# Optimization experiments

Hardware: AMD Instinct MI355X
Metric: run time of the kernel (lower is better)

## Reference

```python
import jax, jax.numpy as jnp
import numpy as np

B, S, H, NH, DH, I, C, P = 4, 1024, 1280, 20, 64, 5120, 13, 8
LN_EPS = 1e-5


def setup_inputs() -> dict:
    key = jax.random.key(0)
    ks = jax.random.split(key, 20)
    n = lambda k, shp, s=0.02: (jax.random.normal(k, shp, jnp.float32) * s)
    return {
        "hidden_states": jax.random.normal(ks[0], (B, S, H), jnp.float32),
        "attention_mask": jnp.ones((B, S), jnp.float32),
        "Wq": n(ks[1], (H, H)), "bq": jnp.zeros((H,), jnp.float32),
        "Wk": n(ks[2], (H, H)), "bk": jnp.zeros((H,), jnp.float32),
        "Wv": n(ks[3], (H, H)), "bv": jnp.zeros((H,), jnp.float32),
        "W_ct1": n(ks[4], (P, C), 0.3), "b_ct1": jnp.zeros((P,), jnp.float32),
        "W_ct2": n(ks[5], (P, C), 0.3), "b_ct2": jnp.zeros((P,), jnp.float32),
        "M": n(ks[6], (C, C), 0.5),
        "bias_scale": jnp.full((1,), 0.5, jnp.float32),
        "W_ptm": n(ks[7], (P, H)), "b_ptm": jnp.zeros((P,), jnp.float32),
        "ln_g": jnp.ones((H,), jnp.float32), "ln_b": jnp.zeros((H,), jnp.float32),
        "Wf1": n(ks[8], (I, H)), "bf1": jnp.zeros((I,), jnp.float32),
        "Wf2": n(ks[9], (H, I)), "bf2": jnp.zeros((H,), jnp.float32),
    }


def reference(hidden_states, attention_mask, Wq, bq, Wk, bk, Wv, bv,
              W_ct1, b_ct1, W_ct2, b_ct2, M, bias_scale, W_ptm, b_ptm,
              ln_g, ln_b, Wf1, bf1, Wf2, bf2):
    h = hidden_states
    # crosstalk bilinear projection: (P,C) @ (C,P) -> (P,P)
    out1 = (M.T @ W_ct1.T + b_ct1).T          # (P, C)
    out2 = M @ W_ct2.T + b_ct2                # (C, P)
    R = out1 @ out2                           # (P, P)
    # ptm_predictor (Linear H->P) + softmax
    ptm = jax.nn.softmax(h @ W_ptm.T + b_ptm, axis=-1)            # (B,S,P)
    Bb = jnp.tanh(jnp.einsum('blc,cd,bmd->blm', ptm, R, ptm)) * bias_scale  # (B,S,S)
    # manual multi-head attention
    q = (h @ Wq.T + bq).reshape(B, S, NH, DH).transpose(0, 2, 1, 3)
    k = (h @ Wk.T + bk).reshape(B, S, NH, DH).transpose(0, 2, 1, 3)
    v = (h @ Wv.T + bv).reshape(B, S, NH, DH).transpose(0, 2, 1, 3)
    scores = jnp.einsum('bhld,bhmd->bhlm', q, k) / np.float32(np.sqrt(DH))
    scores = scores + Bb[:, None]
    scores = scores + (1.0 - attention_mask)[:, None, None, :] * jnp.finfo(h.dtype).min
    probs = jax.nn.softmax(scores, axis=-1)
    ctx = jnp.einsum('bhlm,bhmd->bhld', probs, v)
    ctx = ctx.transpose(0, 2, 1, 3).reshape(B, S, H)
    # residual + LayerNorm
    x = h + ctx
    mu = jnp.mean(x, -1, keepdims=True)
    var = jnp.var(x, -1, keepdims=True)
    x = (x - mu) * jax.lax.rsqrt(var + LN_EPS) * ln_g + ln_b
    # FFN with exact GELU, residual
    ff = jax.nn.gelu(x @ Wf1.T + bf1, approximate=False) @ Wf2.T + bf2
    return x + ff
```

## Files before the change

### kernel.cpp

```cpp
#include <hip/hip_runtime.h>
#include <math.h>

typedef _Float16 f16;
typedef _Float16 f16x2 __attribute__((ext_vector_type(2)));
typedef _Float16 f16x8 __attribute__((ext_vector_type(8)));
typedef _Float16 f16x4 __attribute__((ext_vector_type(4)));
typedef float f32x4 __attribute__((ext_vector_type(4)));

#define B_ 4
#define S_ 1024
#define H_ 1280
#define NH_ 20
#define DH_ 64
#define I_ 5120
#define C_ 13
#define P_ 8
#define LOG2E 1.44269504088896f

__device__ __forceinline__ void store_val(float* p, float v) { *p = v; }
__device__ __forceinline__ void store_val(f16* p, float v) { *p = (f16)v; }

__global__ __launch_bounds__(256) void cvt6_kernel(
    const float* __restrict__ s0, f16* __restrict__ d0, int n0,
    const float* __restrict__ s1, f16* __restrict__ d1, int n1,
    const float* __restrict__ s2, f16* __restrict__ d2, int n2,
    const float* __restrict__ s3, f16* __restrict__ d3, int n3,
    const float* __restrict__ s4, f16* __restrict__ d4, int n4,
    const float* __restrict__ s5, f16* __restrict__ d5, int n5) {
    int seg = blockIdx.y;
    const float* src = (seg == 0) ? s0 : (seg == 1) ? s1 : (seg == 2) ? s2
                     : (seg == 3) ? s3 : (seg == 4) ? s4 : s5;
    f16* dst = (seg == 0) ? d0 : (seg == 1) ? d1 : (seg == 2) ? d2
             : (seg == 3) ? d3 : (seg == 4) ? d4 : d5;
    int n = (seg == 0) ? n0 : (seg == 1) ? n1 : (seg == 2) ? n2
          : (seg == 3) ? n3 : (seg == 4) ? n4 : n5;
    int i = blockIdx.x * 256 + threadIdx.x;
    if (i < n) {
        f32x4 v = ((const f32x4*)src)[i];
        f16x4 o;
#pragma unroll
        for (int e = 0; e < 4; e++) o[e] = (f16)v[e];
        ((f16x4*)dst)[i] = o;
    }
}

__global__ __launch_bounds__(256) void ptm_kernel(const float* __restrict__ hin,
                                                  const float* __restrict__ Wptm,
                                                  const float* __restrict__ bptm,
                                                  const float* __restrict__ Mg,
                                                  const float* __restrict__ W1,
                                                  const float* __restrict__ b1,
                                                  const float* __restrict__ W2,
                                                  const float* __restrict__ b2,
                                                  float* __restrict__ ptm,
                                                  float* __restrict__ tg) {
    __shared__ float o1[P_][C_];
    __shared__ float o2[C_][P_];
    __shared__ float R[P_ * P_];
    int t = threadIdx.x;
    if (t < P_ * C_) {
        int p = t / C_, c = t % C_;
        float s = b1[p];
        for (int k = 0; k < C_; k++) s += Mg[k * C_ + c] * W1[p * C_ + k];
        o1[p][c] = s;
        int c2 = t / P_, p2 = t % P_;
        float s2 = b2[p2];
        for (int k = 0; k < C_; k++) s2 += Mg[c2 * C_ + k] * W2[p2 * C_ + k];
        o2[c2][p2] = s2;
    }
    __syncthreads();
    if (t < P_ * P_) {
        int p = t >> 3, q = t & 7;
        float s = 0.f;
        for (int c = 0; c < C_; c++) s += o1[p][c] * o2[c][q];
        R[t] = s;
    }
    __syncthreads();

    int wv = t >> 6, lane = t & 63;
    int row = blockIdx.x * 4 + wv;
    const float* hrow = hin + (size_t)row * H_;
    float acc[P_] = {};
    for (int i = 0; i < H_ / 64; i++) {
        int k = lane + 64 * i;
        float hv = hrow[k];
#pragma unroll
        for (int p = 0; p < P_; p++) acc[p] += hv * Wptm[p * H_ + k];
    }
#pragma unroll
    for (int p = 0; p < P_; p++) {
#pragma unroll
        for (int o = 32; o >= 1; o >>= 1) acc[p] += __shfl_xor(acc[p], o);
        acc[p] += bptm[p];
    }
    float mx = acc[0];
#pragma unroll
    for (int p = 1; p < P_; p++) mx = fmaxf(mx, acc[p]);
    float sum = 0.f;
#pragma unroll
    for (int p = 0; p < P_; p++) { acc[p] = expf(acc[p] - mx); sum += acc[p]; }
    float rinv = 1.f / sum;
#pragma unroll
    for (int p = 0; p < P_; p++) acc[p] *= rinv;
    float tv[P_];
#pragma unroll
    for (int d = 0; d < P_; d++) {
        float s = 0.f;
#pragma unroll
        for (int c = 0; c < P_; c++) s += acc[c] * R[c * P_ + d];
        tv[d] = s;
    }
    if (lane == 0) {
#pragma unroll
        for (int p = 0; p < P_; p++) {
            ptm[(size_t)row * P_ + p] = acc[p];
            tg[(size_t)row * P_ + p]  = tv[p];
        }
    }
}

__global__ __launch_bounds__(256) void bias_kernel(const float* __restrict__ tg,
                                                   const float* __restrict__ ptm,
                                                   const float* __restrict__ mask,
                                                   const float* __restrict__ bscale_p,
                                                   f16* __restrict__ bb) {
    const int bl = blockIdx.x;
    const int b = bl >> 10;
    const int t = threadIdx.x;
    __shared__ float tl[P_];
    if (t < P_) tl[t] = tg[(size_t)bl * P_ + t];
    __syncthreads();
    const float bscale = bscale_p[0];
    float t0 = tl[0], t1 = tl[1], t2 = tl[2], t3 = tl[3];
    float t4 = tl[4], t5 = tl[5], t6 = tl[6], t7 = tl[7];
#pragma unroll
    for (int i = 0; i < 4; i++) {
        int m = t + 256 * i;
        const float* pm = ptm + ((size_t)b * S_ + m) * P_;
        float4 p0 = *(const float4*)pm;
        float4 p1 = *(const float4*)(pm + 4);
        float d = t0 * p0.x + t1 * p0.y + t2 * p0.z + t3 * p0.w
                + t4 * p1.x + t5 * p1.y + t6 * p1.z + t7 * p1.w;
        float v = (tanhf(d) * bscale + (1.0f - mask[(size_t)b * S_ + m]) * (-30000.0f)) * LOG2E;
        bb[(size_t)bl * S_ + m] = (f16)v;
    }
}

template <int MODE, typename YT>
__device__ __forceinline__ void gemm_body(const f16* __restrict__ X,
                                          const f16* __restrict__ W,
                                          const float* __restrict__ bias,
                                          YT* __restrict__ Y,
                                          const f16* __restrict__ res,
                                          int Ndim, int Kdim, int kbeg, int kend,
                                          int m0, int n0, f16* sA, f16* sB) {
    const int t = threadIdx.x;
    const int lane = t & 63, w = t >> 6;
    const int wr = w >> 1, wc = w & 1;
    const int lr = lane & 15, kq = lane >> 4;

    f32x4 acc[4][4] = {};

    int s_row[4], s_gc[4];
#pragma unroll
    for (int inst = 0; inst < 4; inst++) {
        int ci = t + 256 * inst;
        s_row[inst] = ci >> 3;
        s_gc[inst] = (ci & 7) ^ (s_row[inst] & 7);
    }

    for (int k0 = kbeg; k0 < kend; k0 += 64) {
        __syncthreads();
#pragma unroll
        for (int inst = 0; inst < 4; inst++) {
            int ci = t + 256 * inst;
            __builtin_amdgcn_global_load_lds(
                (const unsigned*)(X + (size_t)(m0 + s_row[inst]) * Kdim + k0 + s_gc[inst] * 8),
                (unsigned*)(sA + ci * 8), 16, 0, 0);
        }
#pragma unroll
        for (int inst = 0; inst < 4; inst++) {
            int ci = t + 256 * inst;
            __builtin_amdgcn_global_load_lds(
                (const unsigned*)(W + (size_t)(n0 + s_row[inst]) * Kdim + k0 + s_gc[inst] * 8),
                (unsigned*)(sB + ci * 8), 16, 0, 0);
        }
        __syncthreads();
#pragma unroll
        for (int ks = 0; ks < 2; ks++) {
            f16x8 af[4], bf[4];
#pragma unroll
            for (int i = 0; i < 4; i++) {
                int row = wr * 64 + i * 16 + lr;
                int cl = (ks * 4 + kq) ^ (row & 7);
                af[i] = *(const f16x8*)(sA + row * 64 + cl * 8);
            }
#pragma unroll
            for (int j = 0; j < 4; j++) {
                int row = wc * 64 + j * 16 + lr;
                int cl = (ks * 4 + kq) ^ (row & 7);
                bf[j] = *(const f16x8*)(sB + row * 64 + cl * 8);
            }
#pragma unroll
            for (int i = 0; i < 4; i++)
#pragma unroll
                for (int j = 0; j < 4; j++)
                    acc[i][j] = __builtin_amdgcn_mfma_f32_16x16x32_f16(af[i], bf[j], acc[i][j], 0, 0, 0);
        }
    }
#pragma unroll
    for (int j = 0; j < 4; j++) {
        int col = n0 + wc * 64 + j * 16 + lr;
        float bcol = (MODE == 3) ? 0.f : bias[col];
#pragma unroll
        for (int i = 0; i < 4; i++) {
#pragma unroll
            for (int rr = 0; rr < 4; rr++) {
                int row = m0 + wr * 64 + i * 16 + kq * 4 + rr;
                float v = acc[i][j][rr] + bcol;
                if (MODE == 1) v = 0.5f * v * (1.0f + erff(v * 0.70710678118654752f));
                if (MODE == 2) v += (float)res[(size_t)row * Ndim + col];
                store_val(&Y[(size_t)row * Ndim + col], v);
            }
        }
    }
}

template <int MODE, typename YT>
__global__ __launch_bounds__(256, 2) void gemm128(const f16* __restrict__ X,
                                                  const f16* __restrict__ W,
                                                  const float* __restrict__ bias,
                                                  YT* __restrict__ Y,
                                                  const f16* __restrict__ res,
                                                  int Ndim, int Kdim) {
    __shared__ f16 sA[128 * 64];
    __shared__ f16 sB[128 * 64];
    gemm_body<MODE, YT>(X, W, bias, Y, res, Ndim, Kdim, 0, Kdim,
                        blockIdx.x * 128, blockIdx.y * 128, sA, sB);
}

__global__ __launch_bounds__(256, 2) void gemm_sk(const f16* __restrict__ X,
                                                  const f16* __restrict__ W,
                                                  float* __restrict__ Pb,
                                                  int Ndim, int Kdim, int Mdim) {
    __shared__ f16 sA[128 * 64];
    __shared__ f16 sB[128 * 64];
    const int kd2 = Kdim >> 1;
    float* Y = Pb + (size_t)blockIdx.z * Mdim * Ndim;
    gemm_body<3, float>(X, W, nullptr, Y, nullptr, Ndim, Kdim,
                        blockIdx.z * kd2, blockIdx.z * kd2 + kd2,
                        blockIdx.x * 128, blockIdx.y * 128, sA, sB);
}

__global__ __launch_bounds__(256) void reduce2_kernel(const float* __restrict__ p0,
                                                      const float* __restrict__ p1,
                                                      const float* __restrict__ bias,
                                                      const f16* __restrict__ res,
                                                      float* __restrict__ out) {
    int i = blockIdx.x * 256 + threadIdx.x;
    int col = (i * 4) % H_;
    f32x4 a = ((const f32x4*)p0)[i];
    f32x4 b = ((const f32x4*)p1)[i];
    f32x4 bc = *(const f32x4*)(bias + col);
    f16x4 r = ((const f16x4*)res)[i];
    f32x4 o;
#pragma unroll
    for (int e = 0; e < 4; e++) o[e] = a[e] + b[e] + bc[e] + (float)r[e];
    ((f32x4*)out)[i] = o;
}

__global__ __launch_bounds__(256, 2) void gemm_qkv(const f16* __restrict__ X,
                                                   const f16* __restrict__ Wq,
                                                   const f16* __restrict__ Wk,
                                                   const f16* __restrict__ Wv,
                                                   const float* __restrict__ bq,
                                                   const float* __restrict__ bk,
                                                   const float* __restrict__ bv,
                                                   f16* __restrict__ qb,
                                                   f16* __restrict__ kb,
                                                   f16* __restrict__ vb) {
    __shared__ f16 sA[128 * 64];
    __shared__ f16 sB[128 * 64];
    const int g = blockIdx.y / 10, nt = blockIdx.y % 10;
    const f16* W = (g == 0) ? Wq : (g == 1) ? Wk : Wv;
    const float* bias = (g == 0) ? bq : (g == 1) ? bk : bv;
    f16* Y = (g == 0) ? qb : (g == 1) ? kb : vb;
    gemm_body<0, f16>(X, W, bias, Y, nullptr, H_, H_, 0, H_,
                      blockIdx.x * 128, nt * 128, sA, sB);
}

__global__ __launch_bounds__(256) void attn_kernel(const f16* __restrict__ q,
                                                   const f16* __restrict__ k,
                                                   const f16* __restrict__ v,
                                                   const f16* __restrict__ bb,
                                                   const float* __restrict__ hin,
                                                   float* __restrict__ xpre) {
    __shared__ f16 sQ[64 * 72];
    __shared__ f16 sK[64 * 72];
    __shared__ f16 sVT[64 * 72];
    __shared__ f16 sP[64 * 72];

    const int t = threadIdx.x;
    const int w = t >> 6, lane = t & 63;
    const int lr = lane & 15, kq = lane >> 4;
    const int gid = blockIdx.x + 16 * (blockIdx.y + 20 * blockIdx.z);
    const int wk = (gid & 7) * 160 + (gid >> 3);
    const int l0 = (wk & 15) * 64;
    const int hb = wk >> 4;
    const int h = hb % 20, b = hb / 20;
    const size_t base = (size_t)b * S_ * H_ + (size_t)h * DH_;

    const int kr0 = t >> 3, kc8 = (t & 7) * 8;
    const int vr2 = (t >> 3) * 2, vc8 = (t & 7) * 8;
    const int vmsw = vr2 ^ vc8;

    f16x8 kA0 = *(const f16x8*)&k[base + (size_t)kr0 * H_ + kc8];
    f16x8 kA1 = *(const f16x8*)&k[base + (size_t)(kr0 + 32) * H_ + kc8];
    f16x8 vA0 = *(const f16x8*)&v[base + (size_t)vr2 * H_ + vc8];
    f16x8 vA1 = *(const f16x8*)&v[base + (size_t)(vr2 + 1) * H_ + vc8];

    for (int idx = t; idx < 512; idx += 256) {
        int r = idx >> 3, c8 = (idx & 7) * 8;
        f16x8 qv = *(const f16x8*)&q[base + (size_t)(l0 + r) * H_ + c8];
#pragma unroll
        for (int e = 0; e < 8; e++) qv[e] = (f16)((float)qv[e] * (0.125f * LOG2E));
        *(f16x8*)&sQ[r * 72 + c8] = qv;
    }
    __syncthreads();
    f16x8 afq[2];
    afq[0] = *(const f16x8*)&sQ[(w * 16 + lr) * 72 + kq * 8];
    afq[1] = *(const f16x8*)&sQ[(w * 16 + lr) * 72 + 32 + kq * 8];

    f32x4 acc_o[4] = {};
    float lstate[4] = {};

    for (int mt = 0; mt < 16; mt++) {
        const int m0 = mt * 64;
        __syncthreads();
        *(f16x8*)&sK[kr0 * 72 + kc8] = kA0;
        *(f16x8*)&sK[(kr0 + 32) * 72 + kc8] = kA1;
#pragma unroll
        for (int e = 0; e < 8; e++) {
            f16x2 pk = {vA0[e], vA1[e]};
            *(f16x2*)&sVT[(vc8 + e) * 72 + vmsw] = pk;
        }
        const int m1 = ((mt + 1) & 15) * 64;
        f16x8 kB0 = *(const f16x8*)&k[base + (size_t)(m1 + kr0) * H_ + kc8];
        f16x8 kB1 = *(const f16x8*)&k[base + (size_t)(m1 + kr0 + 32) * H_ + kc8];
        f16x8 vB0 = *(const f16x8*)&v[base + (size_t)(m1 + vr2) * H_ + vc8];
        f16x8 vB1 = *(const f16x8*)&v[base + (size_t)(m1 + vr2 + 1) * H_ + vc8];
        __syncthreads();

        f32x4 sacc[4] = {};
#pragma unroll
        for (int ks = 0; ks < 2; ks++)
#pragma unroll
            for (int j = 0; j < 4; j++) {
                f16x8 bk = *(const f16x8*)&sK[(j * 16 + lr) * 72 + ks * 32 + kq * 8];
                sacc[j] = __builtin_amdgcn_mfma_f32_16x16x32_f16(afq[ks], bk, sacc[j], 0, 0, 0);
            }
        const f16* bbrow = bb + ((size_t)b * S_ + l0 + w * 16 + kq * 4) * S_ + m0;
#pragma unroll
        for (int j = 0; j < 4; j++)
#pragma unroll
            for (int rr = 0; rr < 4; rr++)
                sacc[j][rr] += (float)bbrow[(size_t)rr * S_ + j * 16 + lr];

#pragma unroll
        for (int j = 0; j < 4; j++)
#pragma unroll
            for (int rr = 0; rr < 4; rr++) {
                float p = __builtin_exp2f(sacc[j][rr]);
                lstate[rr] += p;
                sP[(w * 16 + kq * 4 + rr) * 72 + j * 16 + lr] = (f16)p;
            }
        __syncthreads();

        f16x8 ap[2];
        ap[0] = *(const f16x8*)&sP[(w * 16 + lr) * 72 + kq * 8];
        ap[1] = *(const f16x8*)&sP[(w * 16 + lr) * 72 + 32 + kq * 8];
#pragma unroll
        for (int ks = 0; ks < 2; ks++)
#pragma unroll
            for (int j2 = 0; j2 < 4; j2++) {
                int d = j2 * 16 + lr;
                int s_ = (d >> 3) & 7;
                f16x8 bv = *(const f16x8*)&sVT[d * 72 + 8 * (((ks << 2) + kq) ^ s_)];
                acc_o[j2] = __builtin_amdgcn_mfma_f32_16x16x32_f16(ap[ks], bv, acc_o[j2], 0, 0, 0);
            }
        kA0 = kB0; kA1 = kB1; vA0 = vB0; vA1 = vB1;
    }

#pragma unroll
    for (int rr = 0; rr < 4; rr++) {
#pragma unroll
        for (int off = 8; off >= 1; off >>= 1) lstate[rr] += __shfl_xor(lstate[rr], off);
    }

#pragma unroll
    for (int rr = 0; rr < 4; rr++) {
        float linv = 1.0f / lstate[rr];
        int tok = l0 + w * 16 + kq * 4 + rr;
        size_t obase = base + (size_t)tok * H_;
#pragma unroll
        for (int j2 = 0; j2 < 4; j2++) {
            int d = j2 * 16 + lr;
            xpre[obase + d] = hin[obase + d] + acc_o[j2][rr] * linv;
        }
    }
}

__global__ __launch_bounds__(256) void ln_kernel(const float* __restrict__ xpre,
                                                 const float* __restrict__ g,
                                                 const float* __restrict__ bb,
                                                 f16* __restrict__ xln) {
    int row = blockIdx.x, t = threadIdx.x;
    const float* xr = xpre + (size_t)row * H_;
    float xv[5], s1 = 0.f, s2 = 0.f;
#pragma unroll
    for (int i = 0; i < 5; i++) {
        float v = xr[t + 256 * i];
        xv[i] = v; s1 += v; s2 += v * v;
    }
#pragma unroll
    for (int o = 32; o >= 1; o >>= 1) { s1 += __shfl_xor(s1, o); s2 += __shfl_xor(s2, o); }
    __shared__ float r1[4], r2[4];
    int wv = t >> 6, lane = t & 63;
    if (lane == 0) { r1[wv] = s1; r2[wv] = s2; }
    __syncthreads();
    float m1 = (r1[0] + r1[1] + r1[2] + r1[3]) * (1.0f / H_);
    float m2 = (r2[0] + r2[1] + r2[2] + r2[3]) * (1.0f / H_);
    float rstd = rsqrtf(m2 - m1 * m1 + 1e-5f);
#pragma unroll
    for (int i = 0; i < 5; i++) {
        int c = t + 256 * i;
        float v = (xv[i] - m1) * rstd * g[c] + bb[c];
        xln[(size_t)row * H_ + c] = (f16)v;
    }
}

extern "C" void kernel_launch(void* const* d_in, const int* in_sizes, int n_in,
                              void* d_out, int out_size, void* d_ws, size_t ws_size,
                              hipStream_t stream) {
    (void)in_sizes; (void)n_in; (void)out_size; (void)ws_size;
    const float* hin  = (const float*)d_in[0];
    const float* mask = (const float*)d_in[1];
    const float* Wq = (const float*)d_in[2];  const float* bq = (const float*)d_in[3];
    const float* Wk = (const float*)d_in[4];  const float* bk = (const float*)d_in[5];
    const float* Wv = (const float*)d_in[6];  const float* bv = (const float*)d_in[7];
    const float* Wct1 = (const float*)d_in[8];  const float* bct1 = (const float*)d_in[9];
    const float* Wct2 = (const float*)d_in[10]; const float* bct2 = (const float*)d_in[11];
    const float* Mg = (const float*)d_in[12];   const float* bscale = (const float*)d_in[13];
    const float* Wptm = (const float*)d_in[14]; const float* bptm = (const float*)d_in[15];
    const float* lng = (const float*)d_in[16];  const float* lnb = (const float*)d_in[17];
    const float* Wf1 = (const float*)d_in[18];  const float* bf1 = (const float*)d_in[19];
    const float* Wf2 = (const float*)d_in[20];  const float* bf2 = (const float*)d_in[21];

    char* ws = (char*)d_ws;
    const size_t SZ_PT  = (size_t)B_ * S_ * P_ * 4;
    const size_t SZ_H16 = (size_t)B_ * S_ * H_ * 2;
    const size_t SZ_H32 = (size_t)B_ * S_ * H_ * 4;
    const size_t SZ_WH  = (size_t)H_ * H_ * 2;
    const size_t SZ_WI  = (size_t)I_ * H_ * 2;
    float* ptm  = (float*)(ws + 256);
    float* tg   = (float*)(ws + 256 + SZ_PT);
    char* A0    = ws + 256 + 2 * SZ_PT;
    f16* hin16  = (f16*)(A0);
    f16* qb     = (f16*)(A0 + SZ_H16);
    f16* kb     = (f16*)(A0 + 2 * SZ_H16);
    f16* vb     = (f16*)(A0 + 3 * SZ_H16);
    float* xpre = (float*)(A0 + 4 * SZ_H16);
    f16* xln    = (f16*)(A0 + 4 * SZ_H16 + SZ_H32);
    f16* bbias  = (f16*)(A0 + 5 * SZ_H16 + SZ_H32);
    char* WA    = A0 + 5 * SZ_H16 + SZ_H32 + (size_t)B_ * S_ * S_ * 2;
    f16* Wq16   = (f16*)(WA);
    f16* Wk16   = (f16*)(WA + SZ_WH);
    f16* Wv16   = (f16*)(WA + 2 * SZ_WH);
    f16* Wf116  = (f16*)(WA + 3 * SZ_WH);
    f16* Wf216  = (f16*)(WA + 3 * SZ_WH + SZ_WI);
    f16* g1     = (f16*)(A0);
    float* pbuf = (float*)(WA + 3 * SZ_WH + 2 * SZ_WI);

    const int NH4 = (B_ * S_ * H_) / 4, NW4 = (H_ * H_) / 4, NI4 = (I_ * H_) / 4;
    cvt6_kernel<<<dim3((NI4 + 255) / 256, 6), 256, 0, stream>>>(
        hin, hin16, NH4, Wq, Wq16, NW4, Wk, Wk16, NW4,
        Wv, Wv16, NW4, Wf1, Wf116, NI4, Wf2, Wf216, NI4);

    ptm_kernel<<<S_ * B_ / 4, 256, 0, stream>>>(hin, Wptm, bptm,
                                                Mg, Wct1, bct1, Wct2, bct2, ptm, tg);
    bias_kernel<<<B_ * S_, 256, 0, stream>>>(tg, ptm, mask, bscale, bbias);
    gemm_qkv<<<dim3(32, 30), 256, 0, stream>>>(hin16, Wq16, Wk16, Wv16, bq, bk, bv, qb, kb, vb);
    attn_kernel<<<dim3(S_ / 64, NH_, B_), 256, 0, stream>>>(qb, kb, vb, bbias, hin, xpre);
    ln_kernel<<<B_ * S_, 256, 0, stream>>>(xpre, lng, lnb, xln);
    gemm128<1, f16><<<dim3(32, I_ / 128), 256, 0, stream>>>(xln, Wf116, bf1, g1, nullptr, I_, H_);
    gemm_sk<<<dim3(32, 10, 2), 256, 0, stream>>>(g1, Wf216, pbuf, H_, I_, B_ * S_);
    reduce2_kernel<<<(B_ * S_ * H_) / 4 / 256, 256, 0, stream>>>(
        pbuf, pbuf + (size_t)B_ * S_ * H_, bf2, xln, (float*)d_out);
}
```

Baseline: 482.7 us.

## Prefetch bias tile into shared memory with coalesced loads, drop Q staging

The per-tile attention bias used to be read straight from global memory with scattered 2-byte loads. It is now fetched one tile ahead with coalesced 16-byte loads into registers, stored into the sP shared buffer, and added from shared memory before exp2, which reuses the buffer that later holds the probabilities. Q fragments are loaded directly from global memory into registers, removing the sQ staging buffer and one barrier. s_setprio is raised around the MFMA blocks to favour matrix issue. The risks are extra register pressure from the additional prefetch registers and the need for the shared-memory aliasing of sP to stay correctly synchronized.

```diff
diff --git a/kernel.cpp b/kernel.cpp
--- a/kernel.cpp
+++ b/kernel.cpp
@@ -295,7 +295,6 @@
                                                    const f16* __restrict__ bb,
                                                    const float* __restrict__ hin,
                                                    float* __restrict__ xpre) {
-    __shared__ f16 sQ[64 * 72];
     __shared__ f16 sK[64 * 72];
     __shared__ f16 sVT[64 * 72];
     __shared__ f16 sP[64 * 72];
@@ -313,29 +312,29 @@
     const int kr0 = t >> 3, kc8 = (t & 7) * 8;
     const int vr2 = (t >> 3) * 2, vc8 = (t & 7) * 8;
     const int vmsw = vr2 ^ vc8;
+    const int br = t >> 2, bc16 = (t & 3) * 16;
+    const f16* bbrow0 = bb + ((size_t)b * S_ + l0 + br) * S_;
 
     f16x8 kA0 = *(const f16x8*)&k[base + (size_t)kr0 * H_ + kc8];
     f16x8 kA1 = *(const f16x8*)&k[base + (size_t)(kr0 + 32) * H_ + kc8];
     f16x8 vA0 = *(const f16x8*)&v[base + (size_t)vr2 * H_ + vc8];
     f16x8 vA1 = *(const f16x8*)&v[base + (size_t)(vr2 + 1) * H_ + vc8];
-
-    for (int idx = t; idx < 512; idx += 256) {
-        int r = idx >> 3, c8 = (idx & 7) * 8;
-        f16x8 qv = *(const f16x8*)&q[base + (size_t)(l0 + r) * H_ + c8];
+    f16x8 bA0 = *(const f16x8*)(bbrow0 + bc16);
+    f16x8 bA1 = *(const f16x8*)(bbrow0 + bc16 + 8);
+
+    f16x8 afq[2];
+#pragma unroll
+    for (int ks = 0; ks < 2; ks++) {
+        f16x8 qv = *(const f16x8*)&q[base + (size_t)(l0 + w * 16 + lr) * H_ + ks * 32 + kq * 8];
 #pragma unroll
         for (int e = 0; e < 8; e++) qv[e] = (f16)((float)qv[e] * (0.125f * LOG2E));
-        *(f16x8*)&sQ[r * 72 + c8] = qv;
-    }
-    __syncthreads();
-    f16x8 afq[2];
-    afq[0] = *(const f16x8*)&sQ[(w * 16 + lr) * 72 + kq * 8];
-    afq[1] = *(const f16x8*)&sQ[(w * 16 + lr) * 72 + 32 + kq * 8];
+        afq[ks] = qv;
+    }
 
     f32x4 acc_o[4] = {};
     float lstate[4] = {};
 
     for (int mt = 0; mt < 16; mt++) {
-        const int m0 = mt * 64;
         __syncthreads();
         *(f16x8*)&sK[kr0 * 72 + kc8] = kA0;
         *(f16x8*)&sK[(kr0 + 32) * 72 + kc8] = kA1;
@@ -344,14 +343,19 @@
             f16x2 pk = {vA0[e], vA1[e]};
             *(f16x2*)&sVT[(vc8 + e) * 72 + vmsw] = pk;
         }
+        *(f16x8*)&sP[br * 72 + bc16] = bA0;
+        *(f16x8*)&sP[br * 72 + bc16 + 8] = bA1;
         const int m1 = ((mt + 1) & 15) * 64;
         f16x8 kB0 = *(const f16x8*)&k[base + (size_t)(m1 + kr0) * H_ + kc8];
         f16x8 kB1 = *(const f16x8*)&k[base + (size_t)(m1 + kr0 + 32) * H_ + kc8];
         f16x8 vB0 = *(const f16x8*)&v[base + (size_t)(m1 + vr2) * H_ + vc8];
         f16x8 vB1 = *(const f16x8*)&v[base + (size_t)(m1 + vr2 + 1) * H_ + vc8];
+        f16x8 bB0 = *(const f16x8*)(bbrow0 + m1 + bc16);
+        f16x8 bB1 = *(const f16x8*)(bbrow0 + m1 + bc16 + 8);
         __syncthreads();
 
         f32x4 sacc[4] = {};
+        __builtin_amdgcn_s_setprio(1);
 #pragma unroll
         for (int ks = 0; ks < 2; ks++)
 #pragma unroll
@@ -359,26 +363,23 @@
                 f16x8 bk = *(const f16x8*)&sK[(j * 16 + lr) * 72 + ks * 32 + kq * 8];
                 sacc[j] = __builtin_amdgcn_mfma_f32_16x16x32_f16(afq[ks], bk, sacc[j], 0, 0, 0);
             }
-        const f16* bbrow = bb + ((size_t)b * S_ + l0 + w * 16 + kq * 4) * S_ + m0;
+        __builtin_amdgcn_s_setprio(0);
+
 #pragma unroll
         for (int j = 0; j < 4; j++)
 #pragma unroll
-            for (int rr = 0; rr < 4; rr++)
-                sacc[j][rr] += (float)bbrow[(size_t)rr * S_ + j * 16 + lr];
-
-#pragma unroll
-        for (int j = 0; j < 4; j++)
-#pragma unroll
             for (int rr = 0; rr < 4; rr++) {
-                float p = __builtin_exp2f(sacc[j][rr]);
+                const int sp_addr = (w * 16 + kq * 4 + rr) * 72 + j * 16 + lr;
+                float p = __builtin_exp2f(sacc[j][rr] + (float)sP[sp_addr]);
                 lstate[rr] += p;
-                sP[(w * 16 + kq * 4 + rr) * 72 + j * 16 + lr] = (f16)p;
+                sP[sp_addr] = (f16)p;
             }
         __syncthreads();
 
         f16x8 ap[2];
         ap[0] = *(const f16x8*)&sP[(w * 16 + lr) * 72 + kq * 8];
         ap[1] = *(const f16x8*)&sP[(w * 16 + lr) * 72 + 32 + kq * 8];
+        __builtin_amdgcn_s_setprio(1);
 #pragma unroll
         for (int ks = 0; ks < 2; ks++)
 #pragma unroll
@@ -388,7 +389,8 @@
                 f16x8 bv = *(const f16x8*)&sVT[d * 72 + 8 * (((ks << 2) + kq) ^ s_)];
                 acc_o[j2] = __builtin_amdgcn_mfma_f32_16x16x32_f16(ap[ks], bv, acc_o[j2], 0, 0, 0);
             }
-        kA0 = kB0; kA1 = kB1; vA0 = vB0; vA1 = vB1;
+        __builtin_amdgcn_s_setprio(0);
+        kA0 = kB0; kA1 = kB1; vA0 = vB0; vA1 = vB1; bA0 = bB0; bA1 = bB1;
     }
 
 #pragma unroll
```

New measurement: 452.8 us. 1.07x faster.
